# Kernel optimization log

Measured on AMD Instinct MI355X. Metric: run time of the kernel, lower is better.

## Reference

```python
import jax, jax.numpy as jnp
import numpy as np
import math

B, Q_LEN, PAST, HID = 1, 1024, 3072, 4096
NH, NKV, HD = 32, 8, 128
KV_LEN = PAST + Q_LEN
ROPE_THETA = 10000.0


def setup_inputs() -> dict:
    key = jax.random.key(0)
    ks = jax.random.split(key, 8)
    s = 0.02
    hidden_states = jax.random.normal(ks[0], (B, Q_LEN, HID), jnp.float32)
    # additive causal mask with KV cache offset: query i attends keys j <= PAST + i
    i = jnp.arange(Q_LEN)[:, None]
    j = jnp.arange(KV_LEN)[None, :]
    attention_mask = jnp.where(j <= PAST + i, 0.0, -1e9).astype(jnp.float32)[None, None]
    position_ids = (jnp.arange(Q_LEN, dtype=jnp.int64) + PAST)[None, :]
    past_k = jax.random.normal(ks[1], (B, NKV, PAST, HD), jnp.float32)
    past_v = jax.random.normal(ks[2], (B, NKV, PAST, HD), jnp.float32)
    Wq = jax.random.normal(ks[3], (NH * HD, HID), jnp.float32) * s
    Wk = jax.random.normal(ks[4], (NKV * HD, HID), jnp.float32) * s
    Wv = jax.random.normal(ks[5], (NKV * HD, HID), jnp.float32) * s
    Wo = jax.random.normal(ks[6], (HID, NH * HD), jnp.float32) * s
    return {"hidden_states": hidden_states, "attention_mask": attention_mask,
            "position_ids": position_ids, "past_k": past_k, "past_v": past_v,
            "Wq": Wq, "Wk": Wk, "Wv": Wv, "Wo": Wo}


def _rope_tables(seq_len, head_dim, dtype):
    inv_freq = 1.0 / (ROPE_THETA ** (jnp.arange(0, head_dim, 2, dtype=jnp.float32) / head_dim))
    t = jnp.arange(seq_len, dtype=jnp.float32)
    freqs = jnp.outer(t, inv_freq)            # [seq, hd/2]
    emb = jnp.concatenate([freqs, freqs], -1)  # [seq, hd]
    return jnp.cos(emb).astype(dtype), jnp.sin(emb).astype(dtype)


def _rotate_half(x):
    x1, x2 = jnp.split(x, 2, axis=-1)
    return jnp.concatenate([-x2, x1], axis=-1)


def reference(hidden_states, attention_mask, position_ids, past_k, past_v, Wq, Wk, Wv, Wo):
    bsz, q_len, _ = hidden_states.shape
    q = (hidden_states @ Wq.T).reshape(bsz, q_len, NH, HD).transpose(0, 2, 1, 3)
    k = (hidden_states @ Wk.T).reshape(bsz, q_len, NKV, HD).transpose(0, 2, 1, 3)
    v = (hidden_states @ Wv.T).reshape(bsz, q_len, NKV, HD).transpose(0, 2, 1, 3)

    kv_seq_len = q_len + past_k.shape[2]
    cos_t, sin_t = _rope_tables(kv_seq_len, HD, q.dtype)
    cos = cos_t[position_ids][:, None]  # [b,1,q,hd]
    sin = sin_t[position_ids][:, None]
    q = q * cos + _rotate_half(q) * sin
    k = k * cos + _rotate_half(k) * sin

    k = jnp.concatenate([past_k, k], axis=2)  # [b,nkv,kv,hd]
    v = jnp.concatenate([past_v, v], axis=2)
    n_rep = NH // NKV
    k = jnp.repeat(k, n_rep, axis=1)  # GQA repeat_kv -> [b,nh,kv,hd]
    v = jnp.repeat(v, n_rep, axis=1)

    scores = jnp.einsum('bhqd,bhkd->bhqk', q, k) / math.sqrt(HD)
    scores = scores + attention_mask
    weights = jax.nn.softmax(scores.astype(jnp.float32), axis=-1).astype(q.dtype)
    attn = jnp.einsum('bhqk,bhkd->bhqd', weights, v)
    attn = attn.transpose(0, 2, 1, 3).reshape(bsz, q_len, NH * HD)
    return attn @ Wo.T
```

## Files before the change

### kernel.cpp

```cpp
#include <hip/hip_runtime.h>

#define QLEN 1024
#define PASTN 3072
#define KVLEN 4096
#define HIDN 4096
#define NHEAD 32
#define NKVH 8
#define HDIM 128
#define NQKVC 6144

typedef unsigned short u16;
typedef __bf16 bf16x8 __attribute__((ext_vector_type(8)));
typedef float f32x4 __attribute__((ext_vector_type(4)));
typedef float f32x16 __attribute__((ext_vector_type(16)));
typedef u16 us8 __attribute__((ext_vector_type(8)));
typedef u16 us4 __attribute__((ext_vector_type(4)));

__device__ __forceinline__ u16 f2bf(float x) {
  unsigned u = __builtin_bit_cast(unsigned, x);
  u += 0x7fffu + ((u >> 16) & 1u);
  return (u16)(u >> 16);
}
__device__ __forceinline__ float bf2f(u16 b) {
  return __builtin_bit_cast(float, (unsigned)b << 16);
}

#define GLL16(gp, lp) __builtin_amdgcn_global_load_lds( \
    (const __attribute__((address_space(1))) void*)(gp), \
    (__attribute__((address_space(3))) void*)(lp), 16, 0, 0)

__global__ __launch_bounds__(256) void cvt_kernel(const float* __restrict__ src,
                                                  u16* __restrict__ dst, int n) {
  int i = (blockIdx.x * 256 + threadIdx.x) * 4;
  if (i >= n) return;
  float4 f = *(const float4*)(src + i);
  ushort4 o = make_ushort4(f2bf(f.x), f2bf(f.y), f2bf(f.z), f2bf(f.w));
  *(ushort4*)(dst + i) = o;
}

__device__ __forceinline__ void storeC(float* p, float v) { *p = v; }
__device__ __forceinline__ void storeC(u16* p, float v) { *p = f2bf(v); }

template <typename CT>
__global__ __launch_bounds__(256) void gemm_bt(const u16* __restrict__ A,
                                               const u16* __restrict__ B,
                                               CT* __restrict__ C, int M, int N, int K) {
  __shared__ u16 Alds[2][64 * 32];
  __shared__ u16 Blds[2][128 * 32];
  const int tid = threadIdx.x, wid = tid >> 6, lane = tid & 63;
  const int m0 = blockIdx.y * 64, n0 = blockIdx.x * 128;
  const int wm = (wid >> 1) * 32, wn = (wid & 1) * 64;
  const int l15 = lane & 15, l4 = lane >> 4;
  const int srow = lane >> 2, sp = lane & 3;
  f32x4 acc[2][4] = {};
  auto stage = [&](int buf, int kt) {
    {
      const int r = wid * 16 + srow;
      GLL16(A + (size_t)(m0 + r) * K + kt + (sp ^ ((r >> 1) & 3)) * 8,
            &Alds[buf][wid * 512]);
    }
#pragma unroll
    for (int i = 0; i < 2; ++i) {
      const int c = wid * 2 + i;
      const int r = c * 16 + srow;
      GLL16(B + (size_t)(n0 + r) * K + kt + (sp ^ ((r >> 1) & 3)) * 8,
            &Blds[buf][c * 512]);
    }
  };
  stage(0, 0);
  __syncthreads();
  int cur = 0;
  for (int kt = 0; kt < K; kt += 32) {
    if (kt + 32 < K) stage(cur ^ 1, kt + 32);
    bf16x8 a[2], b[4];
#pragma unroll
    for (int i = 0; i < 2; ++i) {
      const int R = wm + i * 16 + l15;
      a[i] = *(const bf16x8*)&Alds[cur][R * 32 + (l4 ^ ((R >> 1) & 3)) * 8];
    }
#pragma unroll
    for (int j = 0; j < 4; ++j) {
      const int R = wn + j * 16 + l15;
      b[j] = *(const bf16x8*)&Blds[cur][R * 32 + (l4 ^ ((R >> 1) & 3)) * 8];
    }
#pragma unroll
    for (int i = 0; i < 2; ++i)
#pragma unroll
      for (int j = 0; j < 4; ++j)
        acc[i][j] = __builtin_amdgcn_mfma_f32_16x16x32_bf16(a[i], b[j], acc[i][j], 0, 0, 0);
    __syncthreads();
    cur ^= 1;
  }
#pragma unroll
  for (int i = 0; i < 2; ++i)
#pragma unroll
    for (int j = 0; j < 4; ++j) {
      int row = m0 + wm + i * 16 + l4 * 4;
      int col = n0 + wn + j * 16 + l15;
#pragma unroll
      for (int r = 0; r < 4; ++r) storeC(&C[(size_t)(row + r) * N + col], acc[i][j][r]);
    }
}

__global__ __launch_bounds__(256) void rope_q_kernel(const u16* __restrict__ qkv,
                                                     u16* __restrict__ qr) {
  int idx = blockIdx.x * 256 + threadIdx.x;
  int i = idx & 63, h = (idx >> 6) & 31, r = idx >> 11;
  float freq = __expf(-(float)i * (9.210340371976184f / 64.f));
  float angle = (float)(PASTN + r) * freq;
  float sn, cs;
  sincosf(angle, &sn, &cs);
  int base = r * NQKVC + h * HDIM + i;
  float x1 = bf2f(qkv[base]);
  float x2 = bf2f(qkv[base + 64]);
  int ob = r * HIDN + h * HDIM + i;
  qr[ob] = f2bf(x1 * cs - x2 * sn);
  qr[ob + 64] = f2bf(x2 * cs + x1 * sn);
}

__global__ __launch_bounds__(256) void repack_k_kernel(const float* __restrict__ past_k,
                                                       const u16* __restrict__ qkv,
                                                       u16* __restrict__ kb) {
  int idx = blockIdx.x * 256 + threadIdx.x;
  int d = idx & 127, kv = (idx >> 7) & 4095, hk = idx >> 19;
  float val;
  if (kv < PASTN) {
    val = past_k[((size_t)hk * PASTN + kv) * HDIM + d];
  } else {
    int r = kv - PASTN;
    float x = bf2f(qkv[(size_t)r * NQKVC + 4096 + hk * HDIM + d]);
    float xp = bf2f(qkv[(size_t)r * NQKVC + 4096 + hk * HDIM + (d ^ 64)]);
    int i = d & 63;
    float freq = __expf(-(float)i * (9.210340371976184f / 64.f));
    float angle = (float)(PASTN + r) * freq;
    float sn, cs;
    sincosf(angle, &sn, &cs);
    val = (d < 64) ? (x * cs - xp * sn) : (x * cs + xp * sn);
  }
  kb[idx] = f2bf(val);
}

__global__ __launch_bounds__(256) void repack_vt_kernel(const float* __restrict__ past_v,
                                                        const u16* __restrict__ qkv,
                                                        u16* __restrict__ vtb) {
  __shared__ u16 tile[32][136];
  int hk = blockIdx.y, kv0 = blockIdx.x * 32, tid = threadIdx.x;
  int j = tid >> 3, d0 = (tid & 7) * 16;
  if (kv0 < PASTN) {
    const float* src = past_v + ((size_t)hk * PASTN + kv0 + j) * HDIM + d0;
#pragma unroll
    for (int x = 0; x < 16; x += 4) {
      float4 f = *(const float4*)(src + x);
      tile[j][d0 + x] = f2bf(f.x);
      tile[j][d0 + x + 1] = f2bf(f.y);
      tile[j][d0 + x + 2] = f2bf(f.z);
      tile[j][d0 + x + 3] = f2bf(f.w);
    }
  } else {
    int r = kv0 - PASTN + j;
    const u16* src = qkv + (size_t)r * NQKVC + 5120 + hk * HDIM + d0;
    *(us8*)&tile[j][d0] = *(const us8*)src;
    *(us8*)&tile[j][d0 + 8] = *(const us8*)(src + 8);
  }
  __syncthreads();
  int d = tid >> 1, jb = (tid & 1) * 16;
  us8 o0, o1;
#pragma unroll
  for (int x = 0; x < 8; ++x) {
    o0[x] = tile[jb + x][d];
    o1[x] = tile[jb + 8 + x][d];
  }
  u16* dst = vtb + ((size_t)hk * HDIM + d) * KVLEN + kv0 + jb;
  *(us8*)dst = o0;
  *(us8*)(dst + 8) = o1;
}

__global__ __launch_bounds__(512) void attn_kernel(const u16* __restrict__ q,
                                                   const u16* __restrict__ kc,
                                                   const u16* __restrict__ vt,
                                                   float* __restrict__ opart,
                                                   float* __restrict__ mlbuf) {
  __shared__ u16 Klds[2][64 * 128];
  __shared__ u16 Vlds[2][128 * 64];
  const int tid = threadIdx.x, wid = tid >> 6, lane = tid & 63;
  const int l31 = lane & 31, hi = lane >> 5, l15 = lane & 15;
  const int h = blockIdx.y, hk = h >> 2;
  const int q0 = blockIdx.x * 256;
  const int z = blockIdx.z;
  const int pid = h * 4 + blockIdx.x;
  const int qrow = q0 + wid * 32 + l31;
  bf16x8 qf[8];
  {
    const u16* qp = q + (size_t)qrow * HIDN + h * HDIM + hi * 8;
#pragma unroll
    for (int dk = 0; dk < 8; ++dk) qf[dk] = *(const bf16x8*)(qp + dk * 16);
  }
  float m_run = -1e30f, l_run = 0.f;
  f32x16 oacc[4] = {};
  const u16* kbase = kc + (size_t)hk * KVLEN * HDIM;
  const u16* vbase = vt + (size_t)hk * HDIM * KVLEN;
  const int ntiles = (PASTN + q0 + 256) >> 6;
  const int half = ntiles >> 1;
  const int t0 = z ? half : 0, t1 = z ? ntiles : half;
  const float C = 0.12753102f;
  const int qpos = PASTN + qrow;
  auto stage = [&](int buf, int kv0) {
#pragma unroll
    for (int i = 0; i < 2; ++i) {
      const int w = wid * 2 + i;
      const int p = w * 4 + (lane >> 4);
      const int key = (p & 0x33) | ((p & 4) << 1) | ((p & 8) >> 1);
      const int sl = (lane & 15) ^ (p & 15);
      GLL16(kbase + (size_t)(kv0 + key) * HDIM + sl * 8, &Klds[buf][w * 512]);
    }
#pragma unroll
    for (int i = 0; i < 2; ++i) {
      const int w = wid * 2 + i;
      const int d = w * 8 + (lane >> 3);
      const int sl = (lane & 7) ^ ((lane >> 3) & 7);
      GLL16(vbase + (size_t)d * KVLEN + kv0 + sl * 8, &Vlds[buf][w * 512]);
    }
  };
  stage(0, t0 << 6);
  __syncthreads();
  int cur = 0;
  for (int t = t0; t < t1; ++t) {
    if (t + 1 < t1) stage(cur ^ 1, (t + 1) << 6);
    const int kv0 = t << 6;
    const u16* Kb = Klds[cur];
    const u16* Vb = Vlds[cur];
    f32x16 s[2] = {};
    __builtin_amdgcn_s_setprio(1);
#pragma unroll
    for (int tt = 0; tt < 2; ++tt)
#pragma unroll
      for (int dk = 0; dk < 8; ++dk) {
        const int idx = (tt * 32 + l31) * 128 + (((dk * 2 + hi) ^ l15) * 8);
        bf16x8 kf = *(const bf16x8*)&Kb[idx];
        s[tt] = __builtin_amdgcn_mfma_f32_32x32x16_bf16(kf, qf[dk], s[tt], 0, 0, 0);
      }
    __builtin_amdgcn_s_setprio(0);
    float pm = -1e30f;
    if (kv0 + 63 > PASTN + q0) {
#pragma unroll
      for (int tt = 0; tt < 2; ++tt)
#pragma unroll
        for (int reg = 0; reg < 16; ++reg) {
          const int key = kv0 + tt * 32 + (reg & 7) + 8 * hi + ((reg & 8) << 1);
          float v = s[tt][reg] * C;
          if (key > qpos) v = -1e30f;
          s[tt][reg] = v;
          pm = fmaxf(pm, v);
        }
    } else {
#pragma unroll
      for (int tt = 0; tt < 2; ++tt)
#pragma unroll
        for (int reg = 0; reg < 16; ++reg) {
          float v = s[tt][reg] * C;
          s[tt][reg] = v;
          pm = fmaxf(pm, v);
        }
    }
    pm = fmaxf(pm, __shfl_xor(pm, 32));
    if (!__all(pm <= m_run)) {
      const float mn = fmaxf(m_run, pm);
      const float corr = exp2f(m_run - mn);
      m_run = mn;
      l_run *= corr;
#pragma unroll
      for (int db = 0; db < 4; ++db)
#pragma unroll
        for (int r = 0; r < 16; ++r) oacc[db][r] *= corr;
    }
    float rs = 0.f;
#pragma unroll
    for (int tt = 0; tt < 2; ++tt)
#pragma unroll
      for (int reg = 0; reg < 16; ++reg) {
        const float p = exp2f(s[tt][reg] - m_run);
        s[tt][reg] = p;
        rs += p;
      }
    rs += __shfl_xor(rs, 32);
    l_run += rs;
    __builtin_amdgcn_s_setprio(1);
#pragma unroll
    for (int kc2 = 0; kc2 < 4; ++kc2) {
      bf16x8 pa;
#pragma unroll
      for (int j = 0; j < 8; ++j) pa[j] = (__bf16)s[kc2 >> 1][(kc2 & 1) * 8 + j];
#pragma unroll
      for (int db = 0; db < 4; ++db) {
        const int idx = (db * 32 + l31) * 64 + (((kc2 * 2 + hi) ^ (l31 & 7)) * 8);
        bf16x8 vf = *(const bf16x8*)&Vb[idx];
        oacc[db] = __builtin_amdgcn_mfma_f32_32x32x16_bf16(vf, pa, oacc[db], 0, 0, 0);
      }
    }
    __builtin_amdgcn_s_setprio(0);
    __syncthreads();
    cur ^= 1;
  }
  const int orow = wid * 32 + l31;
  float* op = opart + ((size_t)(z * 128 + pid) * 256 + orow) * 128;
#pragma unroll
  for (int db = 0; db < 4; ++db)
#pragma unroll
    for (int g = 0; g < 4; ++g) {
      f32x4 w4;
#pragma unroll
      for (int j = 0; j < 4; ++j) w4[j] = oacc[db][g * 4 + j];
      *(f32x4*)&op[db * 32 + g * 8 + hi * 4] = w4;
    }
  if (hi == 0) {
    float* mlp = mlbuf + ((size_t)(z * 128 + pid) * 256 + orow) * 2;
    mlp[0] = m_run;
    mlp[1] = l_run;
  }
}

__global__ __launch_bounds__(256) void attn_combine(const float* __restrict__ opart,
                                                    const float* __restrict__ mlbuf,
                                                    u16* __restrict__ o) {
  const int pid = blockIdx.x;
  const int h = pid >> 2, qt = pid & 3;
  const int q2 = threadIdx.x >> 2, dc = (threadIdx.x & 3) * 32;
#pragma unroll
  for (int b = 0; b < 4; ++b) {
    const int q = b * 64 + q2;
    const float* ml0 = mlbuf + ((size_t)pid * 256 + q) * 2;
    const float* ml1 = mlbuf + ((size_t)(128 + pid) * 256 + q) * 2;
    const float m0 = ml0[0], l0 = ml0[1], m1 = ml1[0], l1 = ml1[1];
    const float m = fmaxf(m0, m1);
    const float w0 = exp2f(m0 - m), w1 = exp2f(m1 - m);
    const float inv = 1.f / (w0 * l0 + w1 * l1);
    const float* O0 = opart + ((size_t)pid * 256 + q) * 128 + dc;
    const float* O1 = opart + ((size_t)(128 + pid) * 256 + q) * 128 + dc;
    u16* dst = o + (size_t)(qt * 256 + q) * HIDN + h * HDIM + dc;
#pragma unroll
    for (int x = 0; x < 8; ++x) {
      f32x4 a = *(const f32x4*)(O0 + x * 4);
      f32x4 bb = *(const f32x4*)(O1 + x * 4);
      us4 w4;
#pragma unroll
      for (int j = 0; j < 4; ++j) w4[j] = f2bf((a[j] * w0 + bb[j] * w1) * inv);
      *(us4*)(dst + x * 4) = w4;
    }
  }
}

extern "C" void kernel_launch(void* const* d_in, const int* in_sizes, int n_in,
                              void* d_out, int out_size, void* d_ws, size_t ws_size,
                              hipStream_t stream) {
  (void)in_sizes; (void)n_in; (void)out_size; (void)ws_size;
  const float* hidden = (const float*)d_in[0];
  const float* past_k = (const float*)d_in[3];
  const float* past_v = (const float*)d_in[4];
  const float* Wq = (const float*)d_in[5];
  const float* Wk = (const float*)d_in[6];
  const float* Wv = (const float*)d_in[7];
  const float* Wo = (const float*)d_in[8];
  float* out = (float*)d_out;

  char* w = (char*)d_ws;
  u16* hiddenb = (u16*)w; w += (size_t)QLEN * HIDN * 2;
  u16* wqkv    = (u16*)w; w += (size_t)NQKVC * HIDN * 2;
  u16* wo      = (u16*)w; w += (size_t)HIDN * HIDN * 2;
  u16* qkvraw  = (u16*)w; w += (size_t)QLEN * NQKVC * 2;
  u16* qrope   = (u16*)w; w += (size_t)QLEN * HIDN * 2;
  u16* kbuf    = (u16*)w; w += (size_t)NKVH * KVLEN * HDIM * 2;
  u16* vtbuf   = (u16*)w; w += (size_t)NKVH * HDIM * KVLEN * 2;
  u16* attnb   = (u16*)w; w += (size_t)QLEN * HIDN * 2;
  float* opart = (float*)wqkv;
  float* mlbuf = opart + (size_t)2 * 128 * 256 * 128;

  cvt_kernel<<<(QLEN * HIDN) / 1024, 256, 0, stream>>>(hidden, hiddenb, QLEN * HIDN);
  cvt_kernel<<<(NHEAD * HDIM * HIDN) / 1024, 256, 0, stream>>>(Wq, wqkv, NHEAD * HDIM * HIDN);
  cvt_kernel<<<(NKVH * HDIM * HIDN) / 1024, 256, 0, stream>>>(Wk, wqkv + (size_t)4096 * HIDN,
                                                              NKVH * HDIM * HIDN);
  cvt_kernel<<<(NKVH * HDIM * HIDN) / 1024, 256, 0, stream>>>(Wv, wqkv + (size_t)5120 * HIDN,
                                                              NKVH * HDIM * HIDN);
  cvt_kernel<<<(HIDN * HIDN) / 1024, 256, 0, stream>>>(Wo, wo, HIDN * HIDN);

  gemm_bt<u16><<<dim3(NQKVC / 128, QLEN / 64), 256, 0, stream>>>(hiddenb, wqkv, qkvraw,
                                                                 QLEN, NQKVC, HIDN);

  rope_q_kernel<<<(QLEN * NHEAD * 64) / 256, 256, 0, stream>>>(qkvraw, qrope);
  repack_k_kernel<<<(NKVH * KVLEN * HDIM) / 256, 256, 0, stream>>>(past_k, qkvraw, kbuf);
  repack_vt_kernel<<<dim3(KVLEN / 32, NKVH), 256, 0, stream>>>(past_v, qkvraw, vtbuf);

  attn_kernel<<<dim3(QLEN / 256, NHEAD, 2), 512, 0, stream>>>(qrope, kbuf, vtbuf,
                                                              opart, mlbuf);
  attn_combine<<<128, 256, 0, stream>>>(opart, mlbuf, attnb);

  gemm_bt<float><<<dim3(HIDN / 128, QLEN / 64), 256, 0, stream>>>(attnb, wo, out,
                                                                  QLEN, HIDN, HIDN);
}
```

Measured before the change: 344.6 us.

## Fuse fp32 weight conversion into split-K GEMMs, fold softmax scale into Q, widen attention tiles

The separate weight fp32-to-bf16 conversion kernels are removed. The GEMMs now read fp32 weights directly, convert them in registers and write them to LDS. Both GEMMs use split-K by 2 with a combine kernel to add more blocks. The softmax scale moves into the Q rope kernel so attention skips the per-score multiply, and attention processes 128-key tiles per iteration. The fp32 weight loads double weight bytes read per GEMM, and the split-K partials add extra write and read traffic.

```diff
diff --git a/kernel.cpp b/kernel.cpp
--- a/kernel.cpp
+++ b/kernel.cpp
@@ -38,40 +38,63 @@
   *(ushort4*)(dst + i) = o;
 }
 
-__device__ __forceinline__ void storeC(float* p, float v) { *p = v; }
-__device__ __forceinline__ void storeC(u16* p, float v) { *p = f2bf(v); }
-
-template <typename CT>
-__global__ __launch_bounds__(256) void gemm_bt(const u16* __restrict__ A,
-                                               const u16* __restrict__ B,
-                                               CT* __restrict__ C, int M, int N, int K) {
+__global__ __launch_bounds__(256) void gemm_splitf(const u16* __restrict__ A,
+                                                   const float* __restrict__ b0,
+                                                   const float* __restrict__ b1,
+                                                   const float* __restrict__ b2,
+                                                   float* __restrict__ P,
+                                                   int M, int N, int K, int Ks,
+                                                   int S1, int S2) {
   __shared__ u16 Alds[2][64 * 32];
   __shared__ u16 Blds[2][128 * 32];
   const int tid = threadIdx.x, wid = tid >> 6, lane = tid & 63;
   const int m0 = blockIdx.y * 64, n0 = blockIdx.x * 128;
+  const int z = blockIdx.z, zoff = z * Ks;
+  const u16* Az = A + zoff;
+  const float* bsrc;
+  int rbase;
+  if (n0 < S1)      { bsrc = b0; rbase = n0; }
+  else if (n0 < S2) { bsrc = b1; rbase = n0 - S1; }
+  else              { bsrc = b2; rbase = n0 - S2; }
+  float* Cz = P + (size_t)z * M * N;
   const int wm = (wid >> 1) * 32, wn = (wid & 1) * 64;
   const int l15 = lane & 15, l4 = lane >> 4;
   const int srow = lane >> 2, sp = lane & 3;
+  const int br = tid >> 1, bh = tid & 1;
+  const float* bptr = bsrc + (size_t)(rbase + br) * K + zoff + bh * 16;
+  const int bs0 = ((bh * 2 + 0) ^ ((br >> 1) & 3)) * 8;
+  const int bs1 = ((bh * 2 + 1) ^ ((br >> 1) & 3)) * 8;
   f32x4 acc[2][4] = {};
-  auto stage = [&](int buf, int kt) {
-    {
-      const int r = wid * 16 + srow;
-      GLL16(A + (size_t)(m0 + r) * K + kt + (sp ^ ((r >> 1) & 3)) * 8,
-            &Alds[buf][wid * 512]);
-    }
-#pragma unroll
-    for (int i = 0; i < 2; ++i) {
-      const int c = wid * 2 + i;
-      const int r = c * 16 + srow;
-      GLL16(B + (size_t)(n0 + r) * K + kt + (sp ^ ((r >> 1) & 3)) * 8,
-            &Blds[buf][c * 512]);
-    }
+  f32x4 breg[4];
+  auto loadB = [&](int kt) {
+#pragma unroll
+    for (int i = 0; i < 4; ++i) breg[i] = *(const f32x4*)(bptr + kt + i * 4);
   };
-  stage(0, 0);
+  auto writeB = [&](int buf) {
+    us8 w0, w1;
+#pragma unroll
+    for (int j = 0; j < 4; ++j) {
+      w0[j] = __builtin_bit_cast(u16, (__bf16)breg[0][j]);
+      w0[4 + j] = __builtin_bit_cast(u16, (__bf16)breg[1][j]);
+      w1[j] = __builtin_bit_cast(u16, (__bf16)breg[2][j]);
+      w1[4 + j] = __builtin_bit_cast(u16, (__bf16)breg[3][j]);
+    }
+    *(us8*)&Blds[buf][br * 32 + bs0] = w0;
+    *(us8*)&Blds[buf][br * 32 + bs1] = w1;
+  };
+  auto stageA = [&](int buf, int kt) {
+    const int r = wid * 16 + srow;
+    GLL16(Az + (size_t)(m0 + r) * K + kt + (sp ^ ((r >> 1) & 3)) * 8,
+          &Alds[buf][wid * 512]);
+  };
+  loadB(0);
+  stageA(0, 0);
+  writeB(0);
   __syncthreads();
   int cur = 0;
-  for (int kt = 0; kt < K; kt += 32) {
-    if (kt + 32 < K) stage(cur ^ 1, kt + 32);
+  for (int kt = 0; kt < Ks; kt += 32) {
+    const bool more = (kt + 32 < Ks);
+    if (more) { loadB(kt + 32); stageA(cur ^ 1, kt + 32); }
     bf16x8 a[2], b[4];
 #pragma unroll
     for (int i = 0; i < 2; ++i) {
@@ -88,6 +111,7 @@
 #pragma unroll
       for (int j = 0; j < 4; ++j)
         acc[i][j] = __builtin_amdgcn_mfma_f32_16x16x32_bf16(a[i], b[j], acc[i][j], 0, 0, 0);
+    if (more) writeB(cur ^ 1);
     __syncthreads();
     cur ^= 1;
   }
@@ -98,12 +122,35 @@
       int row = m0 + wm + i * 16 + l4 * 4;
       int col = n0 + wn + j * 16 + l15;
 #pragma unroll
-      for (int r = 0; r < 4; ++r) storeC(&C[(size_t)(row + r) * N + col], acc[i][j][r]);
-    }
+      for (int r = 0; r < 4; ++r) Cz[(size_t)(row + r) * N + col] = acc[i][j][r];
+    }
+}
+
+__global__ __launch_bounds__(256) void comb2_bf16(const float* __restrict__ P,
+                                                  u16* __restrict__ C, size_t MN) {
+  const size_t i = ((size_t)blockIdx.x * 256 + threadIdx.x) * 4;
+  f32x4 a = *(const f32x4*)(P + i);
+  f32x4 b = *(const f32x4*)(P + MN + i);
+  us4 o;
+#pragma unroll
+  for (int j = 0; j < 4; ++j) o[j] = f2bf(a[j] + b[j]);
+  *(us4*)(C + i) = o;
+}
+
+__global__ __launch_bounds__(256) void comb2_f32(const float* __restrict__ P,
+                                                 float* __restrict__ C, size_t MN) {
+  const size_t i = ((size_t)blockIdx.x * 256 + threadIdx.x) * 4;
+  f32x4 a = *(const f32x4*)(P + i);
+  f32x4 b = *(const f32x4*)(P + MN + i);
+  f32x4 o;
+#pragma unroll
+  for (int j = 0; j < 4; ++j) o[j] = a[j] + b[j];
+  *(f32x4*)(C + i) = o;
 }
 
 __global__ __launch_bounds__(256) void rope_q_kernel(const u16* __restrict__ qkv,
                                                      u16* __restrict__ qr) {
+  const float SC = 0.12753102f;
   int idx = blockIdx.x * 256 + threadIdx.x;
   int i = idx & 63, h = (idx >> 6) & 31, r = idx >> 11;
   float freq = __expf(-(float)i * (9.210340371976184f / 64.f));
@@ -114,8 +161,8 @@
   float x1 = bf2f(qkv[base]);
   float x2 = bf2f(qkv[base + 64]);
   int ob = r * HIDN + h * HDIM + i;
-  qr[ob] = f2bf(x1 * cs - x2 * sn);
-  qr[ob + 64] = f2bf(x2 * cs + x1 * sn);
+  qr[ob] = f2bf((x1 * cs - x2 * sn) * SC);
+  qr[ob + 64] = f2bf((x2 * cs + x1 * sn) * SC);
 }
 
 __global__ __launch_bounds__(256) void repack_k_kernel(const float* __restrict__ past_k,
@@ -180,8 +227,8 @@
                                                    const u16* __restrict__ vt,
                                                    float* __restrict__ opart,
                                                    float* __restrict__ mlbuf) {
-  __shared__ u16 Klds[2][64 * 128];
-  __shared__ u16 Vlds[2][128 * 64];
+  __shared__ u16 Klds[2][2][64 * 128];
+  __shared__ u16 Vlds[2][2][128 * 64];
   const int tid = threadIdx.x, wid = tid >> 6, lane = tid & 63;
   const int l31 = lane & 31, hi = lane >> 5, l15 = lane & 15;
   const int h = blockIdx.y, hk = h >> 2;
@@ -201,66 +248,70 @@
   const u16* vbase = vt + (size_t)hk * HDIM * KVLEN;
   const int ntiles = (PASTN + q0 + 256) >> 6;
   const int half = ntiles >> 1;
-  const int t0 = z ? half : 0, t1 = z ? ntiles : half;
-  const float C = 0.12753102f;
+  const int base64 = z ? half : 0;
+  const int nt128 = half >> 1;
   const int qpos = PASTN + qrow;
   auto stage = [&](int buf, int kv0) {
 #pragma unroll
-    for (int i = 0; i < 2; ++i) {
-      const int w = wid * 2 + i;
-      const int p = w * 4 + (lane >> 4);
-      const int key = (p & 0x33) | ((p & 4) << 1) | ((p & 8) >> 1);
-      const int sl = (lane & 15) ^ (p & 15);
-      GLL16(kbase + (size_t)(kv0 + key) * HDIM + sl * 8, &Klds[buf][w * 512]);
-    }
-#pragma unroll
-    for (int i = 0; i < 2; ++i) {
-      const int w = wid * 2 + i;
-      const int d = w * 8 + (lane >> 3);
-      const int sl = (lane & 7) ^ ((lane >> 3) & 7);
-      GLL16(vbase + (size_t)d * KVLEN + kv0 + sl * 8, &Vlds[buf][w * 512]);
+    for (int sub = 0; sub < 2; ++sub) {
+#pragma unroll
+      for (int i = 0; i < 2; ++i) {
+        const int w = wid * 2 + i;
+        const int p = w * 4 + (lane >> 4);
+        const int key = (p & 0x33) | ((p & 4) << 1) | ((p & 8) >> 1);
+        const int sl = (lane & 15) ^ (p & 15);
+        GLL16(kbase + (size_t)(kv0 + sub * 64 + key) * HDIM + sl * 8,
+              &Klds[buf][sub][w * 512]);
+      }
+#pragma unroll
+      for (int i = 0; i < 2; ++i) {
+        const int w = wid * 2 + i;
+        const int d = w * 8 + (lane >> 3);
+        const int sl = (lane & 7) ^ ((lane >> 3) & 7);
+        GLL16(vbase + (size_t)d * KVLEN + kv0 + sub * 64 + sl * 8,
+              &Vlds[buf][sub][w * 512]);
+      }
     }
   };
-  stage(0, t0 << 6);
+  stage(0, base64 << 6);
   __syncthreads();
   int cur = 0;
-  for (int t = t0; t < t1; ++t) {
-    if (t + 1 < t1) stage(cur ^ 1, (t + 1) << 6);
-    const int kv0 = t << 6;
-    const u16* Kb = Klds[cur];
-    const u16* Vb = Vlds[cur];
-    f32x16 s[2] = {};
+  for (int t = 0; t < nt128; ++t) {
+    const int kv0 = (base64 << 6) + (t << 7);
+    if (t + 1 < nt128) stage(cur ^ 1, kv0 + 128);
+    f32x16 s[4] = {};
     __builtin_amdgcn_s_setprio(1);
 #pragma unroll
-    for (int tt = 0; tt < 2; ++tt)
-#pragma unroll
-      for (int dk = 0; dk < 8; ++dk) {
-        const int idx = (tt * 32 + l31) * 128 + (((dk * 2 + hi) ^ l15) * 8);
-        bf16x8 kf = *(const bf16x8*)&Kb[idx];
-        s[tt] = __builtin_amdgcn_mfma_f32_32x32x16_bf16(kf, qf[dk], s[tt], 0, 0, 0);
-      }
+    for (int sub = 0; sub < 2; ++sub)
+#pragma unroll
+      for (int tt = 0; tt < 2; ++tt)
+#pragma unroll
+        for (int dk = 0; dk < 8; ++dk) {
+          const int idx = (tt * 32 + l31) * 128 + (((dk * 2 + hi) ^ l15) * 8);
+          bf16x8 kf = *(const bf16x8*)&Klds[cur][sub][idx];
+          s[sub * 2 + tt] =
+              __builtin_amdgcn_mfma_f32_32x32x16_bf16(kf, qf[dk], s[sub * 2 + tt], 0, 0, 0);
+        }
     __builtin_amdgcn_s_setprio(0);
     float pm = -1e30f;
-    if (kv0 + 63 > PASTN + q0) {
-#pragma unroll
-      for (int tt = 0; tt < 2; ++tt)
-#pragma unroll
-        for (int reg = 0; reg < 16; ++reg) {
-          const int key = kv0 + tt * 32 + (reg & 7) + 8 * hi + ((reg & 8) << 1);
-          float v = s[tt][reg] * C;
-          if (key > qpos) v = -1e30f;
-          s[tt][reg] = v;
-          pm = fmaxf(pm, v);
-        }
+    if (kv0 + 127 > PASTN + q0) {
+#pragma unroll
+      for (int sub = 0; sub < 2; ++sub)
+#pragma unroll
+        for (int tt = 0; tt < 2; ++tt)
+#pragma unroll
+          for (int reg = 0; reg < 16; ++reg) {
+            const int key = kv0 + sub * 64 + tt * 32 + (reg & 7) + 8 * hi + ((reg & 8) << 1);
+            float v = s[sub * 2 + tt][reg];
+            if (key > qpos) v = -1e30f;
+            s[sub * 2 + tt][reg] = v;
+            pm = fmaxf(pm, v);
+          }
     } else {
 #pragma unroll
-      for (int tt = 0; tt < 2; ++tt)
-#pragma unroll
-        for (int reg = 0; reg < 16; ++reg) {
-          float v = s[tt][reg] * C;
-          s[tt][reg] = v;
-          pm = fmaxf(pm, v);
-        }
+      for (int x = 0; x < 4; ++x)
+#pragma unroll
+        for (int reg = 0; reg < 16; ++reg) pm = fmaxf(pm, s[x][reg]);
     }
     pm = fmaxf(pm, __shfl_xor(pm, 32));
     if (!__all(pm <= m_run)) {
@@ -275,28 +326,31 @@
     }
     float rs = 0.f;
 #pragma unroll
-    for (int tt = 0; tt < 2; ++tt)
+    for (int x = 0; x < 4; ++x)
 #pragma unroll
       for (int reg = 0; reg < 16; ++reg) {
-        const float p = exp2f(s[tt][reg] - m_run);
-        s[tt][reg] = p;
+        const float p = exp2f(s[x][reg] - m_run);
+        s[x][reg] = p;
         rs += p;
       }
     rs += __shfl_xor(rs, 32);
     l_run += rs;
     __builtin_amdgcn_s_setprio(1);
 #pragma unroll
-    for (int kc2 = 0; kc2 < 4; ++kc2) {
-      bf16x8 pa;
-#pragma unroll
-      for (int j = 0; j < 8; ++j) pa[j] = (__bf16)s[kc2 >> 1][(kc2 & 1) * 8 + j];
-#pragma unroll
-      for (int db = 0; db < 4; ++db) {
-        const int idx = (db * 32 + l31) * 64 + (((kc2 * 2 + hi) ^ (l31 & 7)) * 8);
-        bf16x8 vf = *(const bf16x8*)&Vb[idx];
-        oacc[db] = __builtin_amdgcn_mfma_f32_32x32x16_bf16(vf, pa, oacc[db], 0, 0, 0);
+    for (int sub = 0; sub < 2; ++sub)
+#pragma unroll
+      for (int kc2 = 0; kc2 < 4; ++kc2) {
+        bf16x8 pa;
+#pragma unroll
+        for (int j = 0; j < 8; ++j)
+          pa[j] = (__bf16)s[sub * 2 + (kc2 >> 1)][(kc2 & 1) * 8 + j];
+#pragma unroll
+        for (int db = 0; db < 4; ++db) {
+          const int idx = (db * 32 + l31) * 64 + (((kc2 * 2 + hi) ^ (l31 & 7)) * 8);
+          bf16x8 vf = *(const bf16x8*)&Vlds[cur][sub][idx];
+          oacc[db] = __builtin_amdgcn_mfma_f32_32x32x16_bf16(vf, pa, oacc[db], 0, 0, 0);
+        }
       }
-    }
     __builtin_amdgcn_s_setprio(0);
     __syncthreads();
     cur ^= 1;
@@ -364,26 +418,21 @@
 
   char* w = (char*)d_ws;
   u16* hiddenb = (u16*)w; w += (size_t)QLEN * HIDN * 2;
-  u16* wqkv    = (u16*)w; w += (size_t)NQKVC * HIDN * 2;
-  u16* wo      = (u16*)w; w += (size_t)HIDN * HIDN * 2;
   u16* qkvraw  = (u16*)w; w += (size_t)QLEN * NQKVC * 2;
   u16* qrope   = (u16*)w; w += (size_t)QLEN * HIDN * 2;
   u16* kbuf    = (u16*)w; w += (size_t)NKVH * KVLEN * HDIM * 2;
   u16* vtbuf   = (u16*)w; w += (size_t)NKVH * HDIM * KVLEN * 2;
   u16* attnb   = (u16*)w; w += (size_t)QLEN * HIDN * 2;
-  float* opart = (float*)wqkv;
+  float* gpart = (float*)w;
+  float* opart = (float*)w;
   float* mlbuf = opart + (size_t)2 * 128 * 256 * 128;
+  const size_t MN1 = (size_t)QLEN * NQKVC, MN2 = (size_t)QLEN * HIDN;
 
   cvt_kernel<<<(QLEN * HIDN) / 1024, 256, 0, stream>>>(hidden, hiddenb, QLEN * HIDN);
-  cvt_kernel<<<(NHEAD * HDIM * HIDN) / 1024, 256, 0, stream>>>(Wq, wqkv, NHEAD * HDIM * HIDN);
-  cvt_kernel<<<(NKVH * HDIM * HIDN) / 1024, 256, 0, stream>>>(Wk, wqkv + (size_t)4096 * HIDN,
-                                                              NKVH * HDIM * HIDN);
-  cvt_kernel<<<(NKVH * HDIM * HIDN) / 1024, 256, 0, stream>>>(Wv, wqkv + (size_t)5120 * HIDN,
-                                                              NKVH * HDIM * HIDN);
-  cvt_kernel<<<(HIDN * HIDN) / 1024, 256, 0, stream>>>(Wo, wo, HIDN * HIDN);
-
-  gemm_bt<u16><<<dim3(NQKVC / 128, QLEN / 64), 256, 0, stream>>>(hiddenb, wqkv, qkvraw,
-                                                                 QLEN, NQKVC, HIDN);
+
+  gemm_splitf<<<dim3(NQKVC / 128, QLEN / 64, 2), 256, 0, stream>>>(
+      hiddenb, Wq, Wk, Wv, gpart, QLEN, NQKVC, HIDN, HIDN / 2, 4096, 5120);
+  comb2_bf16<<<(int)(MN1 / 1024), 256, 0, stream>>>(gpart, qkvraw, MN1);
 
   rope_q_kernel<<<(QLEN * NHEAD * 64) / 256, 256, 0, stream>>>(qkvraw, qrope);
   repack_k_kernel<<<(NKVH * KVLEN * HDIM) / 256, 256, 0, stream>>>(past_k, qkvraw, kbuf);
@@ -393,6 +442,7 @@
                                                               opart, mlbuf);
   attn_combine<<<128, 256, 0, stream>>>(opart, mlbuf, attnb);
 
-  gemm_bt<float><<<dim3(HIDN / 128, QLEN / 64), 256, 0, stream>>>(attnb, wo, out,
-                                                                  QLEN, HIDN, HIDN);
-}
+  gemm_splitf<<<dim3(HIDN / 128, QLEN / 64, 2), 256, 0, stream>>>(
+      attnb, Wo, Wo, Wo, gpart, QLEN, HIDN, HIDN, HIDN / 2, HIDN, 2 * HIDN);
+  comb2_f32<<<(int)(MN2 / 1024), 256, 0, stream>>>(gpart, out, MN2);
+}
```

Result: slower. 429.9 us (+24.8%).
